# Performance work log

Measured on AMD Instinct MI355X. Metric: run time of the kernel, lower is better.

The kernel has to match this reference:

```python
import jax, jax.numpy as jnp
import numpy as np

BT, NV, NB, NS, H, W = 8, 10000, 16384, 4096, 256, 256


def setup_inputs() -> dict:
    key = jax.random.key(0)
    k1, k2, k3, k4 = jax.random.split(key, 4)
    verts = jax.random.normal(k1, (BT, NV, 3), dtype=jnp.float32)
    bds_v = jax.random.normal(k2, (BT, NB, 3), dtype=jnp.float32)
    # last channel of bds is a {0,1} mask over boundary samples
    bds_m = (jax.random.uniform(k3, (BT, NB, 1)) > 0.5).astype(jnp.float32)
    bds = jnp.concatenate([bds_v, bds_m], axis=-1)  # [bt, nb, 4]
    pix_to_face = jnp.zeros((BT, H, W, 1), dtype=jnp.int32)  # only shape is used upstream
    # deterministic replacement for torch.randperm(nb)[:n_samples]
    indices = jax.random.permutation(k4, NB)[:NS].astype(jnp.int64)
    return {"verts": verts, "bds": bds, "pix_to_face": pix_to_face, "indices": indices}


def reference(verts, bds, pix_to_face, indices):
    # sample boundary points and mask
    bds_v = bds[:, indices, :-1]          # [bt, ns, 3]
    bds_m = bds[:, indices, -1]           # [bt, ns]
    # squared euclidean distances (= torch.cdist(...)**2): [bt, ns, nv]
    sq_b = jnp.sum(bds_v * bds_v, axis=-1)              # [bt, ns]
    sq_v = jnp.sum(verts * verts, axis=-1)              # [bt, nv]
    cross = jnp.einsum('bsd,bvd->bsv', bds_v, verts)    # [bt, ns, nv]
    dist = sq_b[:, :, None] + sq_v[:, None, :] - 2.0 * cross
    # topk(k=1, largest=False) == min over verts
    min_dists = jnp.min(dist, axis=-1)                   # [bt, ns]
    # (min_dists * mask).mean over k (=1) and samples, then over batch (reduce=True)
    loss = jnp.mean(min_dists * bds_m, axis=-1)          # [bt]
    return jnp.mean(loss)
```

## Files before the change

kernel.cpp:

```cpp
#include <hip/hip_runtime.h>
#include <float.h>

#define BT 8
#define NV 10000
#define NB 16384
#define NS 4096
#define NPTS (BT * NS)
#define PTS_PER_BLOCK 1024
#define SBLOCKS (NPTS / PTS_PER_BLOCK)
#define TILE 2048

__global__ void __launch_bounds__(256, 4)
stage1(const float* __restrict__ verts, const float4* __restrict__ bds4,
       const int* __restrict__ idx, float* __restrict__ pmin,
       int vchunks, int ch) {
    __shared__ float4 sv[TILE];
    const int sblk  = blockIdx.x % SBLOCKS;
    const int chunk = blockIdx.x / SBLOCKS;
    const int b  = sblk * PTS_PER_BLOCK / NS;
    const int p0 = sblk * PTS_PER_BLOCK;
    const int v0 = chunk * ch;
    const int vend = (v0 + ch < NV) ? (v0 + ch) : NV;

    float bx[4], by[4], bz[4], m[4];
#pragma unroll
    for (int k = 0; k < 4; ++k) {
        int pt = p0 + threadIdx.x + k * 256;
        int s = pt & (NS - 1);
        int j = idx[s];
        float4 bp = bds4[(size_t)b * NB + j];
        bx[k] = bp.x; by[k] = bp.y; bz[k] = bp.z;
        m[k] = FLT_MAX;
    }

    for (int t0 = v0; t0 < vend; t0 += TILE) {
        int tn = (TILE < vend - t0) ? TILE : (vend - t0);
        __syncthreads();
        for (int i = threadIdx.x; i < tn; i += 256) {
            const float* vp = verts + (size_t)(b * NV + t0 + i) * 3;
            float x = vp[0], y = vp[1], z = vp[2];
            sv[i] = make_float4(-2.0f * x, -2.0f * y, -2.0f * z,
                                x * x + y * y + z * z);
        }
        __syncthreads();
#pragma unroll 4
        for (int v = 0; v < tn; ++v) {
            float4 q = sv[v];
#pragma unroll
            for (int k = 0; k < 4; ++k) {
                float t = fmaf(bx[k], q.x, fmaf(by[k], q.y, fmaf(bz[k], q.z, q.w)));
                m[k] = fminf(m[k], t);
            }
        }
    }

#pragma unroll
    for (int k = 0; k < 4; ++k) {
        int pt = p0 + threadIdx.x + k * 256;
        pmin[(size_t)chunk * NPTS + pt] = m[k];
    }
}

__global__ void stage2(const float* __restrict__ pmin, const float4* __restrict__ bds4,
                       const int* __restrict__ idx, float* __restrict__ bsum,
                       int vchunks) {
    int pt = blockIdx.x * 256 + threadIdx.x;
    int b = pt >> 12;
    int s = pt & (NS - 1);
    int j = idx[s];
    float4 bp = bds4[(size_t)b * NB + j];
    float md = FLT_MAX;
    for (int c = 0; c < vchunks; ++c)
        md = fminf(md, pmin[(size_t)c * NPTS + pt]);
    float sqb = bp.x * bp.x + bp.y * bp.y + bp.z * bp.z;
    float val = (md + sqb) * bp.w * (1.0f / (float)NPTS);

    for (int o = 32; o > 0; o >>= 1) val += __shfl_down(val, o, 64);
    __shared__ float red[4];
    if ((threadIdx.x & 63) == 0) red[threadIdx.x >> 6] = val;
    __syncthreads();
    if (threadIdx.x == 0) bsum[blockIdx.x] = red[0] + red[1] + red[2] + red[3];
}

__global__ void stage3(const float* __restrict__ bsum, float* __restrict__ out) {
    float v = bsum[threadIdx.x];
    for (int o = 32; o > 0; o >>= 1) v += __shfl_down(v, o, 64);
    __shared__ float r[2];
    if ((threadIdx.x & 63) == 0) r[threadIdx.x >> 6] = v;
    __syncthreads();
    if (threadIdx.x == 0) out[0] = r[0] + r[1];
}

extern "C" void kernel_launch(void* const* d_in, const int* in_sizes, int n_in,
                              void* d_out, int out_size, void* d_ws, size_t ws_size,
                              hipStream_t stream) {
    const float*  verts = (const float*)d_in[0];
    const float4* bds4  = (const float4*)d_in[1];
    const int*    idx   = (const int*)d_in[3];
    float* out = (float*)d_out;

    char* ws = (char*)d_ws;
    size_t per_chunk = (size_t)NPTS * sizeof(float);
    size_t rem = (ws_size > 4096) ? (ws_size - 4096) : 0;
    int vchunks = (int)(rem / per_chunk);
    if (vchunks > 32) vchunks = 32;
    if (vchunks < 1)  vchunks = 1;
    float* pmin = (float*)ws;
    float* bsum = (float*)(ws + (size_t)vchunks * per_chunk);

    int ch = (NV + vchunks - 1) / vchunks;

    stage1<<<SBLOCKS * vchunks, 256, 0, stream>>>(verts, bds4, idx, pmin, vchunks, ch);
    stage2<<<NPTS / 256, 256, 0, stream>>>(pmin, bds4, idx, bsum, vchunks);
    stage3<<<1, 128, 0, stream>>>(bsum, out);
}
```

Measured before the change: 42.97 us.

## Use packed FMA and min3 in distance loop, double points per thread

```diff
diff --git a/kernel.cpp b/kernel.cpp
--- a/kernel.cpp
+++ b/kernel.cpp
@@ -6,58 +6,94 @@
 #define NB 16384
 #define NS 4096
 #define NPTS (BT * NS)
-#define PTS_PER_BLOCK 1024
+#define PTS_PER_BLOCK 2048
 #define SBLOCKS (NPTS / PTS_PER_BLOCK)
-#define TILE 2048
+#define MAXCH 320
+
+typedef float v2f __attribute__((ext_vector_type(2)));
+
+__device__ __forceinline__ v2f pk_fma(v2f a, v2f b, v2f c) {
+    v2f d;
+    asm("v_pk_fma_f32 %0, %1, %2, %3" : "=v"(d) : "v"(a), "v"(b), "v"(c));
+    return d;
+}
+__device__ __forceinline__ float min3f(float a, float b, float c) {
+    float d;
+    asm("v_min3_f32 %0, %1, %2, %3" : "=v"(d) : "v"(a), "v"(b), "v"(c));
+    return d;
+}
 
 __global__ void __launch_bounds__(256, 4)
 stage1(const float* __restrict__ verts, const float4* __restrict__ bds4,
-       const int* __restrict__ idx, float* __restrict__ pmin,
-       int vchunks, int ch) {
-    __shared__ float4 sv[TILE];
+       const int* __restrict__ idx, float* __restrict__ pmin, int ch) {
+    __shared__ float4 sv[2 * MAXCH];
     const int sblk  = blockIdx.x % SBLOCKS;
     const int chunk = blockIdx.x / SBLOCKS;
-    const int b  = sblk * PTS_PER_BLOCK / NS;
+    const int b  = sblk >> 1;
     const int p0 = sblk * PTS_PER_BLOCK;
     const int v0 = chunk * ch;
     const int vend = (v0 + ch < NV) ? (v0 + ch) : NV;
 
-    float bx[4], by[4], bz[4], m[4];
+    v2f bx[4], by[4], bz[4], m[4];
 #pragma unroll
-    for (int k = 0; k < 4; ++k) {
-        int pt = p0 + threadIdx.x + k * 256;
-        int s = pt & (NS - 1);
-        int j = idx[s];
-        float4 bp = bds4[(size_t)b * NB + j];
-        bx[k] = bp.x; by[k] = bp.y; bz[k] = bp.z;
-        m[k] = FLT_MAX;
+    for (int pp = 0; pp < 4; ++pp) {
+        int pt0 = p0 + threadIdx.x + (2 * pp) * 256;
+        int pt1 = pt0 + 256;
+        float4 q0 = bds4[(size_t)b * NB + idx[pt0 & (NS - 1)]];
+        float4 q1 = bds4[(size_t)b * NB + idx[pt1 & (NS - 1)]];
+        bx[pp] = (v2f){q0.x, q1.x};
+        by[pp] = (v2f){q0.y, q1.y};
+        bz[pp] = (v2f){q0.z, q1.z};
+        m[pp]  = (v2f){FLT_MAX, FLT_MAX};
     }
 
-    for (int t0 = v0; t0 < vend; t0 += TILE) {
-        int tn = (TILE < vend - t0) ? TILE : (vend - t0);
+    for (int t0 = v0; t0 < vend; t0 += MAXCH) {
+        const int tn = (MAXCH < vend - t0) ? MAXCH : (vend - t0);
         __syncthreads();
         for (int i = threadIdx.x; i < tn; i += 256) {
             const float* vp = verts + (size_t)(b * NV + t0 + i) * 3;
             float x = vp[0], y = vp[1], z = vp[2];
-            sv[i] = make_float4(-2.0f * x, -2.0f * y, -2.0f * z,
-                                x * x + y * y + z * z);
+            float s = x * x + y * y + z * z;
+            float nx = -2.0f * x, ny = -2.0f * y, nz = -2.0f * z;
+            sv[2 * i]     = make_float4(nx, nx, ny, ny);
+            sv[2 * i + 1] = make_float4(nz, nz, s, s);
         }
         __syncthreads();
-#pragma unroll 4
-        for (int v = 0; v < tn; ++v) {
-            float4 q = sv[v];
+
+        int v = 0;
+        for (; v + 2 <= tn; v += 2) {
+            float4 a0 = sv[2 * v],     b0 = sv[2 * v + 1];
+            float4 a1 = sv[2 * v + 2], b1 = sv[2 * v + 3];
+            v2f qx0 = {a0.x, a0.y}, qy0 = {a0.z, a0.w};
+            v2f qz0 = {b0.x, b0.y}, qw0 = {b0.z, b0.w};
+            v2f qx1 = {a1.x, a1.y}, qy1 = {a1.z, a1.w};
+            v2f qz1 = {b1.x, b1.y}, qw1 = {b1.z, b1.w};
 #pragma unroll
-            for (int k = 0; k < 4; ++k) {
-                float t = fmaf(bx[k], q.x, fmaf(by[k], q.y, fmaf(bz[k], q.z, q.w)));
-                m[k] = fminf(m[k], t);
+            for (int pp = 0; pp < 4; ++pp) {
+                v2f t0v = pk_fma(bx[pp], qx0, pk_fma(by[pp], qy0, pk_fma(bz[pp], qz0, qw0)));
+                v2f t1v = pk_fma(bx[pp], qx1, pk_fma(by[pp], qy1, pk_fma(bz[pp], qz1, qw1)));
+                m[pp].x = min3f(m[pp].x, t0v.x, t1v.x);
+                m[pp].y = min3f(m[pp].y, t0v.y, t1v.y);
+            }
+        }
+        if (v < tn) {
+            float4 a0 = sv[2 * v], b0 = sv[2 * v + 1];
+            v2f qx0 = {a0.x, a0.y}, qy0 = {a0.z, a0.w};
+            v2f qz0 = {b0.x, b0.y}, qw0 = {b0.z, b0.w};
+#pragma unroll
+            for (int pp = 0; pp < 4; ++pp) {
+                v2f t0v = pk_fma(bx[pp], qx0, pk_fma(by[pp], qy0, pk_fma(bz[pp], qz0, qw0)));
+                m[pp].x = fminf(m[pp].x, t0v.x);
+                m[pp].y = fminf(m[pp].y, t0v.y);
             }
         }
     }
 
 #pragma unroll
-    for (int k = 0; k < 4; ++k) {
-        int pt = p0 + threadIdx.x + k * 256;
-        pmin[(size_t)chunk * NPTS + pt] = m[k];
+    for (int pp = 0; pp < 4; ++pp) {
+        int pt0 = p0 + threadIdx.x + (2 * pp) * 256;
+        pmin[(size_t)chunk * NPTS + pt0]       = m[pp].x;
+        pmin[(size_t)chunk * NPTS + pt0 + 256] = m[pp].y;
     }
 }
 
@@ -103,14 +139,14 @@
     size_t per_chunk = (size_t)NPTS * sizeof(float);
     size_t rem = (ws_size > 4096) ? (ws_size - 4096) : 0;
     int vchunks = (int)(rem / per_chunk);
-    if (vchunks > 32) vchunks = 32;
+    if (vchunks > 64) vchunks = 64;
     if (vchunks < 1)  vchunks = 1;
     float* pmin = (float*)ws;
     float* bsum = (float*)(ws + (size_t)vchunks * per_chunk);
 
     int ch = (NV + vchunks - 1) / vchunks;
 
-    stage1<<<SBLOCKS * vchunks, 256, 0, stream>>>(verts, bds4, idx, pmin, vchunks, ch);
+    stage1<<<SBLOCKS * vchunks, 256, 0, stream>>>(verts, bds4, idx, pmin, ch);
     stage2<<<NPTS / 256, 256, 0, stream>>>(pmin, bds4, idx, bsum, vchunks);
     stage3<<<1, 128, 0, stream>>>(bsum, out);
 }
```

Result: slower. 51.32 us (+19.4%).

## Raise register blocking to 8 points per thread and fuse mins with v_min3

Applied to the files above, without the earlier changes.

```diff
diff --git a/kernel.cpp b/kernel.cpp
--- a/kernel.cpp
+++ b/kernel.cpp
@@ -6,75 +6,83 @@
 #define NB 16384
 #define NS 4096
 #define NPTS (BT * NS)
-#define PTS_PER_BLOCK 1024
-#define SBLOCKS (NPTS / PTS_PER_BLOCK)
-#define TILE 2048
+#define PTSB 2048
+#define PB (NPTS / PTSB)
+#define VCH 32
+#define CH 313
+#define SVMAX 316
+
+__device__ __forceinline__ float min3f(float a, float b, float c) {
+    float d;
+    asm("v_min3_f32 %0, %1, %2, %3" : "=v"(d) : "v"(a), "v"(b), "v"(c));
+    return d;
+}
 
 __global__ void __launch_bounds__(256, 4)
 stage1(const float* __restrict__ verts, const float4* __restrict__ bds4,
-       const int* __restrict__ idx, float* __restrict__ pmin,
-       int vchunks, int ch) {
-    __shared__ float4 sv[TILE];
-    const int sblk  = blockIdx.x % SBLOCKS;
-    const int chunk = blockIdx.x / SBLOCKS;
-    const int b  = sblk * PTS_PER_BLOCK / NS;
-    const int p0 = sblk * PTS_PER_BLOCK;
-    const int v0 = chunk * ch;
-    const int vend = (v0 + ch < NV) ? (v0 + ch) : NV;
+       const int* __restrict__ idx, float* __restrict__ pmin) {
+    __shared__ float4 sv[SVMAX];
+    const int tid = threadIdx.x;
+    const int pb  = blockIdx.x & (PB - 1);
+    const int c   = blockIdx.x >> 4;
+    const int b   = pb >> 1;
+    const int p0  = pb * PTSB;
+    const int v0  = c * CH;
+    const int vend = (v0 + CH < NV) ? (v0 + CH) : NV;
+    const int tn  = vend - v0;
+    const int tn4 = (tn + 3) & ~3;
 
-    float bx[4], by[4], bz[4], m[4];
+    for (int i = tid; i < tn4; i += 256) {
+        float4 q;
+        if (i < tn) {
+            const float* vp = verts + (size_t)(b * NV + v0 + i) * 3;
+            float x = vp[0], y = vp[1], z = vp[2];
+            q = make_float4(-2.0f * x, -2.0f * y, -2.0f * z, x * x + y * y + z * z);
+        } else {
+            q = make_float4(0.0f, 0.0f, 0.0f, 3.4e38f);
+        }
+        sv[i] = q;
+    }
+
+    float bx[8], by[8], bz[8], m[8];
 #pragma unroll
-    for (int k = 0; k < 4; ++k) {
-        int pt = p0 + threadIdx.x + k * 256;
-        int s = pt & (NS - 1);
-        int j = idx[s];
-        float4 bp = bds4[(size_t)b * NB + j];
+    for (int k = 0; k < 8; ++k) {
+        int pt = p0 + tid + k * 256;
+        float4 bp = bds4[(size_t)b * NB + idx[pt & (NS - 1)]];
         bx[k] = bp.x; by[k] = bp.y; bz[k] = bp.z;
         m[k] = FLT_MAX;
     }
+    __syncthreads();
 
-    for (int t0 = v0; t0 < vend; t0 += TILE) {
-        int tn = (TILE < vend - t0) ? TILE : (vend - t0);
-        __syncthreads();
-        for (int i = threadIdx.x; i < tn; i += 256) {
-            const float* vp = verts + (size_t)(b * NV + t0 + i) * 3;
-            float x = vp[0], y = vp[1], z = vp[2];
-            sv[i] = make_float4(-2.0f * x, -2.0f * y, -2.0f * z,
-                                x * x + y * y + z * z);
-        }
-        __syncthreads();
-#pragma unroll 4
-        for (int v = 0; v < tn; ++v) {
-            float4 q = sv[v];
+    for (int v = 0; v < tn4; v += 4) {
+        float4 q0 = sv[v], q1 = sv[v + 1], q2 = sv[v + 2], q3 = sv[v + 3];
 #pragma unroll
-            for (int k = 0; k < 4; ++k) {
-                float t = fmaf(bx[k], q.x, fmaf(by[k], q.y, fmaf(bz[k], q.z, q.w)));
-                m[k] = fminf(m[k], t);
-            }
+        for (int k = 0; k < 8; ++k) {
+            float t0 = fmaf(bx[k], q0.x, fmaf(by[k], q0.y, fmaf(bz[k], q0.z, q0.w)));
+            float t1 = fmaf(bx[k], q1.x, fmaf(by[k], q1.y, fmaf(bz[k], q1.z, q1.w)));
+            float t2 = fmaf(bx[k], q2.x, fmaf(by[k], q2.y, fmaf(bz[k], q2.z, q2.w)));
+            float t3 = fmaf(bx[k], q3.x, fmaf(by[k], q3.y, fmaf(bz[k], q3.z, q3.w)));
+            m[k] = min3f(m[k], t0, t1);
+            m[k] = min3f(m[k], t2, t3);
         }
     }
 
 #pragma unroll
-    for (int k = 0; k < 4; ++k) {
-        int pt = p0 + threadIdx.x + k * 256;
-        pmin[(size_t)chunk * NPTS + pt] = m[k];
-    }
+    for (int k = 0; k < 8; ++k)
+        pmin[(size_t)c * NPTS + p0 + tid + k * 256] = m[k];
 }
 
 __global__ void stage2(const float* __restrict__ pmin, const float4* __restrict__ bds4,
-                       const int* __restrict__ idx, float* __restrict__ bsum,
-                       int vchunks) {
+                       const int* __restrict__ idx, float* __restrict__ bsum) {
     int pt = blockIdx.x * 256 + threadIdx.x;
-    int b = pt >> 12;
-    int s = pt & (NS - 1);
-    int j = idx[s];
-    float4 bp = bds4[(size_t)b * NB + j];
+    int b = pt >> 12, s = pt & (NS - 1);
+    float4 bp = bds4[(size_t)b * NB + idx[s]];
     float md = FLT_MAX;
-    for (int c = 0; c < vchunks; ++c)
+#pragma unroll 8
+    for (int c = 0; c < VCH; ++c)
         md = fminf(md, pmin[(size_t)c * NPTS + pt]);
     float sqb = bp.x * bp.x + bp.y * bp.y + bp.z * bp.z;
     float val = (md + sqb) * bp.w * (1.0f / (float)NPTS);
-
     for (int o = 32; o > 0; o >>= 1) val += __shfl_down(val, o, 64);
     __shared__ float red[4];
     if ((threadIdx.x & 63) == 0) red[threadIdx.x >> 6] = val;
@@ -100,17 +108,10 @@
     float* out = (float*)d_out;
 
     char* ws = (char*)d_ws;
-    size_t per_chunk = (size_t)NPTS * sizeof(float);
-    size_t rem = (ws_size > 4096) ? (ws_size - 4096) : 0;
-    int vchunks = (int)(rem / per_chunk);
-    if (vchunks > 32) vchunks = 32;
-    if (vchunks < 1)  vchunks = 1;
     float* pmin = (float*)ws;
-    float* bsum = (float*)(ws + (size_t)vchunks * per_chunk);
+    float* bsum = (float*)(ws + (size_t)VCH * NPTS * sizeof(float));
 
-    int ch = (NV + vchunks - 1) / vchunks;
-
-    stage1<<<SBLOCKS * vchunks, 256, 0, stream>>>(verts, bds4, idx, pmin, vchunks, ch);
-    stage2<<<NPTS / 256, 256, 0, stream>>>(pmin, bds4, idx, bsum, vchunks);
+    stage1<<<PB * VCH, 256, 0, stream>>>(verts, bds4, idx, pmin);
+    stage2<<<NPTS / 256, 256, 0, stream>>>(pmin, bds4, idx, bsum);
     stage3<<<1, 128, 0, stream>>>(bsum, out);
 }
```

New measurement: 45.11 us. +5.0%, slower.
